# Performance work log

Measured on AMD Instinct MI355X. Metric: run time of the kernel, lower is better.

## Reference

```python
import jax, jax.numpy as jnp
import numpy as np

SEQ_LENGTH = 4096
HIDDEN = 4096
N_HEADS = 32
N_KV = 2
HEAD_DIM = 128
ROT_DIM = 64  # head_dim // 2, rotary applied to first half
FFN = 13696
EPS = 1e-5


def rope_cache(seq_len):
    theta = 1.0 / (10000.0 ** (jnp.arange(0, ROT_DIM, 2, dtype=jnp.float32) / ROT_DIM))  # [32]
    idx = jnp.arange(seq_len, dtype=jnp.float32)
    freqs = jnp.outer(idx, theta)  # [seq, 32]
    return jnp.stack([jnp.cos(freqs), jnp.sin(freqs)], axis=-1)  # [seq, 32, 2]


def apply_rope(x, rope):
    # x: [sq, b, nh, 128]; rope: [sq, b, 32, 2]
    sq, b, nh, hn = x.shape
    xr = x[..., :ROT_DIM].reshape(sq, b, nh, ROT_DIM // 2, 2)
    x0, x1 = xr[..., 0], xr[..., 1]
    cos = rope[:, :, None, :, 0]
    sin = rope[:, :, None, :, 1]
    out = jnp.stack([x0 * cos - x1 * sin, x1 * cos + x0 * sin], axis=-1)
    out = out.reshape(sq, b, nh, ROT_DIM)
    return jnp.concatenate([out, x[..., ROT_DIM:]], axis=-1)


def rmsnorm(x, w):
    var = jnp.mean(jnp.square(x), axis=-1, keepdims=True)
    return x * jax.lax.rsqrt(var + EPS) * w


def setup_inputs() -> dict:
    key = jax.random.key(0)
    ks = jax.random.split(key, 12)
    B, L = 32, SEQ_LENGTH - 1
    s = 0.02
    return {
        'hidden_states': jax.random.normal(ks[0], (1, B, HIDDEN), jnp.float32),
        'position_ids': jax.random.randint(ks[1], (B, 1), 0, SEQ_LENGTH),
        'attention_mask': jnp.zeros((B, 1, 1, SEQ_LENGTH), dtype=bool),
        'past_k': jax.random.normal(ks[2], (L, B, N_KV, HEAD_DIM), jnp.float32),
        'past_v': jax.random.normal(ks[3], (L, B, N_KV, HEAD_DIM), jnp.float32),
        'w_ln1': 1.0 + s * jax.random.normal(ks[4], (HIDDEN,), jnp.float32),
        'w_qkv': s * jax.random.normal(ks[5], (HIDDEN + 2 * N_KV * HEAD_DIM, HIDDEN), jnp.float32),
        'b_qkv': s * jax.random.normal(ks[6], (HIDDEN + 2 * N_KV * HEAD_DIM,), jnp.float32),
        'w_dense': s * jax.random.normal(ks[7], (HIDDEN, HIDDEN), jnp.float32),
        'w_ln2': 1.0 + s * jax.random.normal(ks[8], (HIDDEN,), jnp.float32),
        'w_fc1': s * jax.random.normal(ks[9], (2 * FFN, HIDDEN), jnp.float32),
        'w_fc2': s * jax.random.normal(ks[10], (HIDDEN, FFN), jnp.float32),
    }


def reference(hidden_states, position_ids, attention_mask, past_k, past_v,
              w_ln1, w_qkv, b_qkv, w_dense, w_ln2, w_fc1, w_fc2):
    sq, B, _ = hidden_states.shape
    # rotary_pos_emb(SEQ_LENGTH)[position_ids].transpose(0, 1)
    rope = rope_cache(SEQ_LENGTH)[position_ids]          # [B, sq, 32, 2]
    rope = jnp.transpose(rope, (1, 0, 2, 3))             # [sq, B, 32, 2]

    # --- self attention ---
    residual = hidden_states
    x = rmsnorm(hidden_states, w_ln1)
    qkv = jnp.einsum('sbh,oh->sbo', x, w_qkv) + b_qkv    # [sq, B, 4608]
    q = qkv[..., :HIDDEN].reshape(sq, B, N_HEADS, HEAD_DIM)
    k = qkv[..., HIDDEN:HIDDEN + N_KV * HEAD_DIM].reshape(sq, B, N_KV, HEAD_DIM)
    v = qkv[..., HIDDEN + N_KV * HEAD_DIM:].reshape(sq, B, N_KV, HEAD_DIM)
    q = apply_rope(q, rope)
    k = apply_rope(k, rope)

    k_cache = jnp.concatenate([past_k, k], axis=0)       # [L+sq, B, 2, 128]
    v_cache = jnp.concatenate([past_v, v], axis=0)

    rep = N_HEADS // N_KV
    kx = jnp.repeat(k_cache, rep, axis=2)                # [sk, B, 32, 128]
    vx = jnp.repeat(v_cache, rep, axis=2)

    scale = 1.0 / jnp.sqrt(jnp.float32(HEAD_DIM))
    scores = jnp.einsum('qbhd,kbhd->bhqk', q, kx) * scale  # [B, 32, sq, sk]
    scores = jnp.where(attention_mask, jnp.float32(-1e9), scores)
    probs = jax.nn.softmax(scores, axis=-1)
    ctx = jnp.einsum('bhqk,kbhd->qbhd', probs, vx).reshape(sq, B, HIDDEN)
    attn_out = jnp.einsum('sbh,oh->sbo', ctx, w_dense)

    hidden = residual + attn_out

    # --- MLP (SwiGLU) ---
    residual = hidden
    x = rmsnorm(hidden, w_ln2)
    h = jnp.einsum('sbh,oh->sbo', x, w_fc1)              # [sq, B, 2*FFN]
    a, b = jnp.split(h, 2, axis=-1)
    h = jax.nn.silu(a) * b
    mlp_out = jnp.einsum('sbf,of->sbo', h, w_fc2)
    hidden = residual + mlp_out

    return hidden, k_cache[1:], v_cache[1:]
```

## Files before the change

### kernel.cpp

```cpp
#include <hip/hip_runtime.h>


constexpr int B    = 32;
constexpr int HID  = 4096;
constexpr int NKV  = 2;
constexpr int HD   = 128;
constexpr int QKVN = 4608;
constexpr int FFN  = 13696;
constexpr int FC1N = 2 * FFN;
constexpr int PAST = 4095;
constexpr int NSPL = 16;

constexpr size_t OFF_X1   = 0;
constexpr size_t OFF_P    = OFF_X1   + (size_t)B * HID;
constexpr size_t P_SIZE   = 2ull * B * FC1N;
constexpr size_t OFF_Q    = OFF_P    + P_SIZE;
constexpr size_t OFF_KN   = OFF_Q    + (size_t)B * HID;
constexpr size_t OFF_VN   = OFF_KN   + (size_t)B * NKV * HD;
constexpr size_t OFF_CTXP = OFF_VN   + (size_t)B * NKV * HD;
constexpr size_t OFF_ML   = OFF_CTXP + (size_t)B * NKV * NSPL * 16 * HD;
constexpr size_t OFF_CTX  = OFF_ML   + (size_t)B * NKV * NSPL * 16 * 2;
constexpr size_t OFF_HID  = OFF_CTX  + (size_t)B * HID;
constexpr size_t OFF_X2   = OFF_HID  + (size_t)B * HID;
constexpr size_t OFF_HG   = OFF_X2   + (size_t)B * HID;

__global__ __launch_bounds__(256) void k_rmsnorm(
    const float* __restrict__ x, const float* __restrict__ w,
    float* __restrict__ out)
{
  const int b = blockIdx.x, t = threadIdx.x;
  const float* xr = x + (size_t)b * HID;
  float4 v[4];
  float ss = 0.f;
#pragma unroll
  for (int r = 0; r < 4; r++) {
    v[r] = *(const float4*)&xr[(t + r * 256) * 4];
    ss += v[r].x * v[r].x + v[r].y * v[r].y + v[r].z * v[r].z + v[r].w * v[r].w;
  }
#pragma unroll
  for (int off = 32; off; off >>= 1) ss += __shfl_xor(ss, off);
  __shared__ float wsum[4];
  if ((t & 63) == 0) wsum[t >> 6] = ss;
  __syncthreads();
  const float tot = wsum[0] + wsum[1] + wsum[2] + wsum[3];
  const float inv = rsqrtf(tot * (1.f / HID) + 1e-5f);
  float* orow = out + (size_t)b * HID;
#pragma unroll
  for (int r = 0; r < 4; r++) {
    const int i = (t + r * 256) * 4;
    const float4 wv = *(const float4*)&w[i];
    float4 o;
    o.x = v[r].x * inv * wv.x;
    o.y = v[r].y * inv * wv.y;
    o.z = v[r].z * inv * wv.z;
    o.w = v[r].w * inv * wv.w;
    *(float4*)&orow[i] = o;
  }
}

__global__ __launch_bounds__(256) void k_resid_norm(
    const float* __restrict__ hs, const float* __restrict__ dpart,
    const float* __restrict__ w, float* __restrict__ hid,
    float* __restrict__ out)
{
  const int b = blockIdx.x, t = threadIdx.x;
  float4 v[4];
  float ss = 0.f;
#pragma unroll
  for (int r = 0; r < 4; r++) {
    const int i = (t + r * 256) * 4;
    float4 a = *(const float4*)&hs[(size_t)b * HID + i];
#pragma unroll
    for (int s = 0; s < 8; s++) {
      const float4 p = *(const float4*)&dpart[((size_t)s * B + b) * HID + i];
      a.x += p.x; a.y += p.y; a.z += p.z; a.w += p.w;
    }
    v[r] = a;
    *(float4*)&hid[(size_t)b * HID + i] = a;
    ss += a.x * a.x + a.y * a.y + a.z * a.z + a.w * a.w;
  }
#pragma unroll
  for (int off = 32; off; off >>= 1) ss += __shfl_xor(ss, off);
  __shared__ float wsum[4];
  if ((t & 63) == 0) wsum[t >> 6] = ss;
  __syncthreads();
  const float tot = wsum[0] + wsum[1] + wsum[2] + wsum[3];
  const float inv = rsqrtf(tot * (1.f / HID) + 1e-5f);
#pragma unroll
  for (int r = 0; r < 4; r++) {
    const int i = (t + r * 256) * 4;
    const float4 wv = *(const float4*)&w[i];
    float4 o;
    o.x = v[r].x * inv * wv.x;
    o.y = v[r].y * inv * wv.y;
    o.z = v[r].z * inv * wv.z;
    o.w = v[r].w * inv * wv.w;
    *(float4*)&out[(size_t)b * HID + i] = o;
  }
}

__global__ __launch_bounds__(256, 2) void k_gemv32(
    const float* __restrict__ A, const float* __restrict__ W,
    const float* __restrict__ bias, float* __restrict__ outp,
    int N, int K, int ksplit_len)
{
  __shared__ __align__(16) float xs[8192];
  const int t = threadIdx.x;
  const int wv = t >> 6, l = t & 63;
  const int olane = l >> 3, kq = l & 7;
  const int o_base = blockIdx.x * 64;
  const int kb = blockIdx.y * ksplit_len;
  const int ke = kb + ksplit_len;

  float acc[8][8];
#pragma unroll
  for (int j = 0; j < 8; j++)
#pragma unroll
    for (int bb = 0; bb < 8; bb++) acc[j][bb] = 0.f;

  const float* W0 = W + (size_t)(o_base + olane) * K;
  const size_t rowstride8 = (size_t)8 * K;

  for (int kc = kb; kc < ke; kc += 256) {
    const int csz = min(256, ke - kc);
    const int c4n = csz >> 2;
    __syncthreads();
#pragma unroll
    for (int r = 0; r < 8; r++) {
      const int f = t + r * 256;
      const int b = f >> 6, c4 = f & 63;
      if (c4 < c4n)
        *(float4*)&xs[b * 256 + c4 * 4] =
            *(const float4*)&A[(size_t)b * K + kc + c4 * 4];
    }
    __syncthreads();
#pragma unroll
    for (int i = 0; i < 8; i++) {
      const int kl = i * 32 + kq * 4;
      if (kl < csz) {
        float4 w4[8];
#pragma unroll
        for (int j = 0; j < 8; j++)
          w4[j] = *(const float4*)&W0[j * rowstride8 + kc + kl];
#pragma unroll
        for (int bb = 0; bb < 8; bb++) {
          const float4 xv = *(const float4*)&xs[(wv * 8 + bb) * 256 + kl];
#pragma unroll
          for (int j = 0; j < 8; j++)
            acc[j][bb] += w4[j].x * xv.x + w4[j].y * xv.y +
                          w4[j].z * xv.z + w4[j].w * xv.w;
        }
      }
    }
  }
#pragma unroll
  for (int j = 0; j < 8; j++)
#pragma unroll
    for (int bb = 0; bb < 8; bb++) {
      float v = acc[j][bb];
      v += __shfl_xor(v, 1);
      v += __shfl_xor(v, 2);
      v += __shfl_xor(v, 4);
      acc[j][bb] = v;
    }
  __syncthreads();
  if (kq == 0) {
#pragma unroll
    for (int j = 0; j < 8; j++)
#pragma unroll
      for (int bb = 0; bb < 8; bb++)
        xs[(olane + 8 * j) * 33 + (wv * 8 + bb)] = acc[j][bb];
  }
  __syncthreads();
#pragma unroll
  for (int r = 0; r < 8; r++) {
    const int pair = t + r * 256;
    const int b = pair >> 6, rl = pair & 63;
    float v = xs[rl * 33 + b];
    if (bias != nullptr && blockIdx.y == 0) v += bias[o_base + rl];
    outp[((size_t)blockIdx.y * B + b) * N + o_base + rl] = v;
  }
}

__global__ __launch_bounds__(256) void k_qkv_rope(
    const float* __restrict__ qkvp, const int* __restrict__ pos_ids,
    float* __restrict__ qo, float* __restrict__ ko, float* __restrict__ vo)
{
  const int idx = blockIdx.x * 256 + threadIdx.x;
  const int b = idx / 1152;
  const int f4 = idx - b * 1152;
  const int o = f4 * 4;
  float4 v = {0.f, 0.f, 0.f, 0.f};
#pragma unroll
  for (int s = 0; s < 8; s++) {
    const float4 p = *(const float4*)&qkvp[((size_t)s * B + b) * QKVN + o];
    v.x += p.x; v.y += p.y; v.z += p.z; v.w += p.w;
  }
  const int d = o & 127;
  if (o < HID + NKV * HD && d < 64) {
    const int pos = pos_ids[b];
    const int i0 = d >> 1;
    const float f0 = pos * __expf(-0.28782313662425572f * i0);
    const float f1 = pos * __expf(-0.28782313662425572f * (i0 + 1));
    float c0, s0, c1, s1;
    sincosf(f0, &s0, &c0);
    sincosf(f1, &s1, &c1);
    float4 r;
    r.x = v.x * c0 - v.y * s0;
    r.y = v.y * c0 + v.x * s0;
    r.z = v.z * c1 - v.w * s1;
    r.w = v.w * c1 + v.z * s1;
    v = r;
  }
  if (o < HID) {
    *(float4*)&qo[(size_t)b * HID + o] = v;
  } else if (o < HID + NKV * HD) {
    *(float4*)&ko[(size_t)b * (NKV * HD) + (o - HID)] = v;
  } else {
    *(float4*)&vo[(size_t)b * (NKV * HD) + (o - HID - NKV * HD)] = v;
  }
}

__global__ __launch_bounds__(256) void k_attn_partial(
    const float* __restrict__ q, const float* __restrict__ past_k,
    const float* __restrict__ past_v, const float* __restrict__ kn,
    const float* __restrict__ vn, float* __restrict__ ok,
    float* __restrict__ ov, float* __restrict__ ctxp,
    float* __restrict__ mlbuf)
{
  __shared__ __align__(16) float qs[16 * 128];
  __shared__ __align__(16) float sc[256 * 20];
  const int t = threadIdx.x;
  const int split = blockIdx.x, kvh = blockIdx.y, b = blockIdx.z;

#pragma unroll
  for (int r = 0; r < 2; r++) {
    const int f4 = t + r * 256;
    const int hh = f4 >> 5, d4 = f4 & 31;
    *(float4*)&qs[hh * 128 + d4 * 4] =
        *(const float4*)&q[(size_t)b * HID + (kvh * 16 + hh) * HD + d4 * 4];
  }

  {
    const int r8 = t >> 5, d4 = t & 31;
#pragma unroll 4
    for (int rr = 0; rr < 32; rr++) {
      const int pg = split * 256 + rr * 8 + r8;
      if (pg >= 1) {
        const float4 kv = (pg < PAST)
            ? *(const float4*)&past_k[(((size_t)pg * B + b) * NKV + kvh) * HD + d4 * 4]
            : *(const float4*)&kn[((size_t)b * NKV + kvh) * HD + d4 * 4];
        *(float4*)&ok[(((size_t)(pg - 1) * B + b) * NKV + kvh) * HD + d4 * 4] = kv;
      }
    }
  }
  __syncthreads();

  const float scale = 0.08838834764831845f;
  {
    const int pl = t;
    const int pg = split * 256 + pl;
    const float* kr = (pg < PAST)
        ? &past_k[(((size_t)pg * B + b) * NKV + kvh) * HD]
        : &kn[((size_t)b * NKV + kvh) * HD];
    float s[16];
#pragma unroll
    for (int hh = 0; hh < 16; hh++) s[hh] = 0.f;
#pragma unroll 4
    for (int d4 = 0; d4 < 32; d4++) {
      const float4 kv = *(const float4*)&kr[d4 * 4];
#pragma unroll
      for (int hh = 0; hh < 16; hh++) {
        const float4 q4 = *(const float4*)&qs[hh * 128 + d4 * 4];
        s[hh] += q4.x * kv.x + q4.y * kv.y + q4.z * kv.z + q4.w * kv.w;
      }
    }
#pragma unroll
    for (int hh = 0; hh < 16; hh++) sc[pl * 20 + hh] = s[hh] * scale;
  }
  __syncthreads();

  {
    const int hh = t >> 4, l16 = t & 15;
    float m = -1e30f;
    for (int jj = 0; jj < 16; jj++)
      m = fmaxf(m, sc[(l16 + jj * 16) * 20 + hh]);
#pragma unroll
    for (int off = 8; off; off >>= 1) m = fmaxf(m, __shfl_xor(m, off));
    float lsum = 0.f;
    for (int jj = 0; jj < 16; jj++) {
      const int p = l16 + jj * 16;
      const float e = __expf(sc[p * 20 + hh] - m);
      sc[p * 20 + hh] = e;
      lsum += e;
    }
#pragma unroll
    for (int off = 8; off; off >>= 1) lsum += __shfl_xor(lsum, off);
    if (l16 == 0) {
      const size_t base =
          (((size_t)(b * NKV + kvh) * NSPL + split) * 16 + hh) * 2;
      mlbuf[base] = m;
      mlbuf[base + 1] = lsum;
    }
  }
  __syncthreads();

  const int hg = t >> 7, d = t & 127;
  float acc[8];
#pragma unroll
  for (int k8 = 0; k8 < 8; k8++) acc[k8] = 0.f;
  for (int pl = 0; pl < 256; pl++) {
    const int pg = split * 256 + pl;
    const float vd = (pg < PAST)
        ? past_v[(((size_t)pg * B + b) * NKV + kvh) * HD + d]
        : vn[((size_t)b * NKV + kvh) * HD + d];
    if (hg == 0 && pg >= 1)
      ov[(((size_t)(pg - 1) * B + b) * NKV + kvh) * HD + d] = vd;
    const float4 e0 = *(const float4*)&sc[pl * 20 + hg * 8];
    const float4 e1 = *(const float4*)&sc[pl * 20 + hg * 8 + 4];
    acc[0] += e0.x * vd; acc[1] += e0.y * vd;
    acc[2] += e0.z * vd; acc[3] += e0.w * vd;
    acc[4] += e1.x * vd; acc[5] += e1.y * vd;
    acc[6] += e1.z * vd; acc[7] += e1.w * vd;
  }
#pragma unroll
  for (int k8 = 0; k8 < 8; k8++) {
    const size_t idx =
        (((size_t)(b * NKV + kvh) * NSPL + split) * 16 + hg * 8 + k8) * HD + d;
    ctxp[idx] = acc[k8];
  }
}

__global__ __launch_bounds__(128) void k_attn_merge(
    const float* __restrict__ ctxp, const float* __restrict__ mlbuf,
    float* __restrict__ ctx)
{
  const int h = blockIdx.x, b = blockIdx.y, d = threadIdx.x;
  const int kvh = h >> 4, hh = h & 15;
  float ms[NSPL], ls[NSPL];
  float M = -1e30f;
#pragma unroll
  for (int s = 0; s < NSPL; s++) {
    const size_t base = (((size_t)(b * NKV + kvh) * NSPL + s) * 16 + hh) * 2;
    ms[s] = mlbuf[base];
    ls[s] = mlbuf[base + 1];
    M = fmaxf(M, ms[s]);
  }
  float L = 0.f, val = 0.f;
#pragma unroll
  for (int s = 0; s < NSPL; s++) {
    const float w = __expf(ms[s] - M);
    L += ls[s] * w;
    val += w * ctxp[(((size_t)(b * NKV + kvh) * NSPL + s) * 16 + hh) * HD + d];
  }
  ctx[(size_t)b * HID + h * HD + d] = val / L;
}

__global__ __launch_bounds__(256) void k_swiglu(
    const float* __restrict__ h1p, float* __restrict__ hg)
{
  const int idx = blockIdx.x * 256 + threadIdx.x;
  const int b = idx / 3424;
  const int f4 = idx - b * 3424;
  float4 a = *(const float4*)&h1p[(size_t)b * FC1N + f4 * 4];
  float4 g = *(const float4*)&h1p[(size_t)b * FC1N + FFN + f4 * 4];
  const float4 a1 = *(const float4*)&h1p[((size_t)B + b) * FC1N + f4 * 4];
  const float4 g1 = *(const float4*)&h1p[((size_t)B + b) * FC1N + FFN + f4 * 4];
  a.x += a1.x; a.y += a1.y; a.z += a1.z; a.w += a1.w;
  g.x += g1.x; g.y += g1.y; g.z += g1.z; g.w += g1.w;
  float4 o;
  o.x = a.x / (1.f + __expf(-a.x)) * g.x;
  o.y = a.y / (1.f + __expf(-a.y)) * g.y;
  o.z = a.z / (1.f + __expf(-a.z)) * g.z;
  o.w = a.w / (1.f + __expf(-a.w)) * g.w;
  *(float4*)&hg[(size_t)b * FFN + f4 * 4] = o;
}

__global__ __launch_bounds__(256) void k_final(
    const float* __restrict__ hid, const float* __restrict__ fp,
    float* __restrict__ out)
{
  const int idx = blockIdx.x * 256 + threadIdx.x;
  const int b = idx >> 10, i4 = idx & 1023;
  float4 v = *(const float4*)&hid[(size_t)b * HID + i4 * 4];
#pragma unroll
  for (int s = 0; s < 8; s++) {
    const float4 p = *(const float4*)&fp[((size_t)s * B + b) * HID + i4 * 4];
    v.x += p.x; v.y += p.y; v.z += p.z; v.w += p.w;
  }
  *(float4*)&out[(size_t)b * HID + i4 * 4] = v;
}

extern "C" void kernel_launch(void* const* d_in, const int* in_sizes, int n_in,
                              void* d_out, int out_size, void* d_ws,
                              size_t ws_size, hipStream_t stream)
{
  const float* hs     = (const float*)d_in[0];
  const int*   pos    = (const int*)  d_in[1];
  const float* pk     = (const float*)d_in[3];
  const float* pv     = (const float*)d_in[4];
  const float* wln1   = (const float*)d_in[5];
  const float* wqkv   = (const float*)d_in[6];
  const float* bqkv   = (const float*)d_in[7];
  const float* wdense = (const float*)d_in[8];
  const float* wln2   = (const float*)d_in[9];
  const float* wfc1   = (const float*)d_in[10];
  const float* wfc2   = (const float*)d_in[11];

  float* ws  = (float*)d_ws;
  float* out = (float*)d_out;

  float* x1    = ws + OFF_X1;
  float* P     = ws + OFF_P;
  float* q     = ws + OFF_Q;
  float* kn    = ws + OFF_KN;
  float* vn    = ws + OFF_VN;
  float* ctxp  = ws + OFF_CTXP;
  float* mlbuf = ws + OFF_ML;
  float* ctx   = ws + OFF_CTX;
  float* hid   = ws + OFF_HID;
  float* x2    = ws + OFF_X2;
  float* hg    = ws + OFF_HG;

  float* out_k = out + (size_t)B * HID;
  float* out_v = out_k + (size_t)PAST * B * NKV * HD;

  hipLaunchKernelGGL(k_rmsnorm, dim3(B), dim3(256), 0, stream, hs, wln1, x1);
  hipLaunchKernelGGL(k_gemv32, dim3(QKVN / 64, 8), dim3(256), 0, stream,
                     x1, wqkv, bqkv, P, QKVN, HID, HID / 8);
  hipLaunchKernelGGL(k_qkv_rope, dim3(144), dim3(256), 0, stream,
                     P, pos, q, kn, vn);
  hipLaunchKernelGGL(k_attn_partial, dim3(NSPL, NKV, B), dim3(256), 0, stream,
                     q, pk, pv, kn, vn, out_k, out_v, ctxp, mlbuf);
  hipLaunchKernelGGL(k_attn_merge, dim3(32, 32), dim3(128), 0, stream,
                     ctxp, mlbuf, ctx);
  hipLaunchKernelGGL(k_gemv32, dim3(HID / 64, 8), dim3(256), 0, stream,
                     ctx, wdense, (const float*)nullptr, P, HID, HID, HID / 8);
  hipLaunchKernelGGL(k_resid_norm, dim3(B), dim3(256), 0, stream,
                     hs, P, wln2, hid, x2);
  hipLaunchKernelGGL(k_gemv32, dim3(FC1N / 64, 2), dim3(256), 0, stream,
                     x2, wfc1, (const float*)nullptr, P, FC1N, HID, HID / 2);
  hipLaunchKernelGGL(k_swiglu, dim3(428), dim3(256), 0, stream, P, hg);
  hipLaunchKernelGGL(k_gemv32, dim3(HID / 64, 8), dim3(256), 0, stream,
                     hg, wfc2, (const float*)nullptr, P, HID, FFN, FFN / 8);
  hipLaunchKernelGGL(k_final, dim3(128), dim3(256), 0, stream, hid, P, out);
}
```

Baseline: 579.2 us.

## Restructure attention PV accumulation to float4 per-thread rows with cross-wave reduction

```diff
diff --git a/kernel.cpp b/kernel.cpp
--- a/kernel.cpp
+++ b/kernel.cpp
@@ -228,29 +228,30 @@
     float* __restrict__ ov, float* __restrict__ ctxp,
     float* __restrict__ mlbuf)
 {
-  __shared__ __align__(16) float qs[16 * 128];
-  __shared__ __align__(16) float sc[256 * 20];
+  __shared__ __align__(16) float smem[8192];
+  float* sc = smem;
+  float* qs = smem + 5120;
   const int t = threadIdx.x;
   const int split = blockIdx.x, kvh = blockIdx.y, b = blockIdx.z;
 
 #pragma unroll
   for (int r = 0; r < 2; r++) {
     const int f4 = t + r * 256;
-    const int hh = f4 >> 5, d4 = f4 & 31;
-    *(float4*)&qs[hh * 128 + d4 * 4] =
-        *(const float4*)&q[(size_t)b * HID + (kvh * 16 + hh) * HD + d4 * 4];
+    const int hh = f4 >> 5, d4q = f4 & 31;
+    *(float4*)&qs[hh * 128 + d4q * 4] =
+        *(const float4*)&q[(size_t)b * HID + (kvh * 16 + hh) * HD + d4q * 4];
   }
 
   {
-    const int r8 = t >> 5, d4 = t & 31;
+    const int r8 = t >> 5, d4c = t & 31;
 #pragma unroll 4
     for (int rr = 0; rr < 32; rr++) {
       const int pg = split * 256 + rr * 8 + r8;
       if (pg >= 1) {
         const float4 kv = (pg < PAST)
-            ? *(const float4*)&past_k[(((size_t)pg * B + b) * NKV + kvh) * HD + d4 * 4]
-            : *(const float4*)&kn[((size_t)b * NKV + kvh) * HD + d4 * 4];
-        *(float4*)&ok[(((size_t)(pg - 1) * B + b) * NKV + kvh) * HD + d4 * 4] = kv;
+            ? *(const float4*)&past_k[(((size_t)pg * B + b) * NKV + kvh) * HD + d4c * 4]
+            : *(const float4*)&kn[((size_t)b * NKV + kvh) * HD + d4c * 4];
+        *(float4*)&ok[(((size_t)(pg - 1) * B + b) * NKV + kvh) * HD + d4c * 4] = kv;
       }
     }
   }
@@ -305,29 +306,54 @@
   }
   __syncthreads();
 
-  const int hg = t >> 7, d = t & 127;
-  float acc[8];
-#pragma unroll
-  for (int k8 = 0; k8 < 8; k8++) acc[k8] = 0.f;
-  for (int pl = 0; pl < 256; pl++) {
+  const int pr = t >> 5, d4 = t & 31;
+  float4 acc[16];
+#pragma unroll
+  for (int hh = 0; hh < 16; hh++) acc[hh] = float4{0.f, 0.f, 0.f, 0.f};
+#pragma unroll 2
+  for (int j = 0; j < 32; j++) {
+    const int pl = pr * 32 + j;
     const int pg = split * 256 + pl;
-    const float vd = (pg < PAST)
-        ? past_v[(((size_t)pg * B + b) * NKV + kvh) * HD + d]
-        : vn[((size_t)b * NKV + kvh) * HD + d];
-    if (hg == 0 && pg >= 1)
-      ov[(((size_t)(pg - 1) * B + b) * NKV + kvh) * HD + d] = vd;
-    const float4 e0 = *(const float4*)&sc[pl * 20 + hg * 8];
-    const float4 e1 = *(const float4*)&sc[pl * 20 + hg * 8 + 4];
-    acc[0] += e0.x * vd; acc[1] += e0.y * vd;
-    acc[2] += e0.z * vd; acc[3] += e0.w * vd;
-    acc[4] += e1.x * vd; acc[5] += e1.y * vd;
-    acc[6] += e1.z * vd; acc[7] += e1.w * vd;
-  }
-#pragma unroll
-  for (int k8 = 0; k8 < 8; k8++) {
-    const size_t idx =
-        (((size_t)(b * NKV + kvh) * NSPL + split) * 16 + hg * 8 + k8) * HD + d;
-    ctxp[idx] = acc[k8];
+    const float4 v4 = (pg < PAST)
+        ? *(const float4*)&past_v[(((size_t)pg * B + b) * NKV + kvh) * HD + d4 * 4]
+        : *(const float4*)&vn[((size_t)b * NKV + kvh) * HD + d4 * 4];
+    if (pg >= 1)
+      *(float4*)&ov[(((size_t)(pg - 1) * B + b) * NKV + kvh) * HD + d4 * 4] = v4;
+#pragma unroll
+    for (int h4 = 0; h4 < 4; h4++) {
+      const float4 e = *(const float4*)&sc[pl * 20 + h4 * 4];
+      acc[h4 * 4 + 0].x += e.x * v4.x; acc[h4 * 4 + 0].y += e.x * v4.y;
+      acc[h4 * 4 + 0].z += e.x * v4.z; acc[h4 * 4 + 0].w += e.x * v4.w;
+      acc[h4 * 4 + 1].x += e.y * v4.x; acc[h4 * 4 + 1].y += e.y * v4.y;
+      acc[h4 * 4 + 1].z += e.y * v4.z; acc[h4 * 4 + 1].w += e.y * v4.w;
+      acc[h4 * 4 + 2].x += e.z * v4.x; acc[h4 * 4 + 2].y += e.z * v4.y;
+      acc[h4 * 4 + 2].z += e.z * v4.z; acc[h4 * 4 + 2].w += e.z * v4.w;
+      acc[h4 * 4 + 3].x += e.w * v4.x; acc[h4 * 4 + 3].y += e.w * v4.y;
+      acc[h4 * 4 + 3].z += e.w * v4.z; acc[h4 * 4 + 3].w += e.w * v4.w;
+    }
+  }
+#pragma unroll
+  for (int hh = 0; hh < 16; hh++) {
+    acc[hh].x += __shfl_xor(acc[hh].x, 32);
+    acc[hh].y += __shfl_xor(acc[hh].y, 32);
+    acc[hh].z += __shfl_xor(acc[hh].z, 32);
+    acc[hh].w += __shfl_xor(acc[hh].w, 32);
+  }
+  __syncthreads();
+  if ((t & 63) < 32) {
+    const int w = t >> 6;
+#pragma unroll
+    for (int hh = 0; hh < 16; hh++)
+      *(float4*)&smem[w * 2048 + hh * 128 + d4 * 4] = acc[hh];
+  }
+  __syncthreads();
+#pragma unroll
+  for (int r = 0; r < 8; r++) {
+    const int o = t + r * 256;
+    const int hh = o >> 7, d = o & 127;
+    const float v = smem[hh * 128 + d] + smem[2048 + hh * 128 + d] +
+                    smem[4096 + hh * 128 + d] + smem[6144 + hh * 128 + d];
+    ctxp[(((size_t)(b * NKV + kvh) * NSPL + split) * 16 + hh) * HD + d] = v;
   }
 }
 
```

Result: faster. 545.0 us (-5.9%).
